# Optimization experiments

Hardware: AMD Instinct MI355X
Metric: run time of the kernel (lower is better)

## Reference

```python
import jax, jax.numpy as jnp
import numpy as np

NUM_EXPERTS = 8
TOP_K = 2
N_EMBD = 1024
D_FFN = 2048  # 4*N_EMBD // TOP_K, already multiple of BLOCK_N=128
BLOCK_M = 128
NORM_TOPK = True


def setup_inputs() -> dict:
    key = jax.random.key(0)
    k1, k2, k3 = jax.random.split(key, 3)
    x = jax.random.normal(k1, (2, 2048, N_EMBD), dtype=jnp.float32)
    router_w = jax.random.normal(k2, (NUM_EXPERTS, N_EMBD), dtype=jnp.float32) * 0.02
    w1 = jax.random.normal(k3, (N_EMBD, D_FFN * NUM_EXPERTS), dtype=jnp.float32) * 0.02
    return {"x": x, "router_w": router_w, "w1": w1}


def reference(x, router_w, w1):
    B, S, H = x.shape
    x_flat = x.reshape(-1, H)                                   # [T, H]
    router_logits = x_flat @ router_w.T                         # [T, E]
    probs = jax.nn.softmax(router_logits.astype(jnp.float32), axis=-1)
    rweights, sel = jax.lax.top_k(probs, TOP_K)                 # [T, k]
    if NORM_TOPK:
        rweights = rweights / rweights.sum(axis=-1, keepdims=True)
    rweights = rweights.astype(x.dtype)

    # repeat_interleave tokens top_k times, then stable-sort by expert id
    x_rep = jnp.repeat(x_flat, TOP_K, axis=0)                   # [M, H]
    sel_rep = sel.reshape(-1)                                   # [M]
    rw_rep = rweights.reshape(-1, 1)                            # [M, 1]
    order = jnp.argsort(sel_rep, stable=True)                   # expert-sort permutation
    x_grouped = x_rep[order]                                    # [M, H]
    sel_sorted = sel_rep[order]                                 # [M]
    rw_sorted = rw_rep[order]                                   # [M, 1]

    M = x_grouped.shape[0]
    nblk = M // BLOCK_M                                         # M divisible by BLOCK_M by construction
    # SDD kernel: expert of the first row of each BLOCK_M block selects w1 slice
    block_expert = sel_sorted[::BLOCK_M]                        # [nblk] == col_indices_ptr
    w1e = w1.reshape(H, NUM_EXPERTS, D_FFN)                     # w1[:, e*D:(e+1)*D] == w1e[:, e, :]
    w_blk = jnp.take(w1e, block_expert, axis=1)                 # [H, nblk, D]
    x_blk = x_grouped.reshape(nblk, BLOCK_M, H)                 # [nblk, Bm, H]
    block_sparse = jnp.einsum('bmh,hbd->bmd', x_blk, w_blk).reshape(M, D_FFN)

    block_sparse = jax.nn.gelu(block_sparse, approximate=False) * rw_sorted
    return block_sparse, router_logits
```

## Files before the change

kernel.cpp:

```cpp
#include <hip/hip_runtime.h>
#include <hip/hip_bf16.h>
#include <cmath>

typedef float f32x16 __attribute__((ext_vector_type(16)));
typedef __bf16 bf16x8 __attribute__((ext_vector_type(8)));
typedef __bf16 bf16x4 __attribute__((ext_vector_type(4)));

#define NE 8
#define H 1024
#define DF 2048
#define WCOLS 16384
#define NTOK 4096
#define MROWS 8192
#define NBLK 64
#define TILE_E 4096

typedef const __attribute__((address_space(1))) unsigned int glb_u32;
typedef __attribute__((address_space(3))) unsigned int lds_u32;

__device__ __forceinline__ void async_load16(const void* g, void* l) {
    __builtin_amdgcn_global_load_lds((glb_u32*)g, (lds_u32*)l, 16, 0, 0);
}

__global__ __launch_bounds__(256) void prep_kernel(
    const float* __restrict__ x, const float* __restrict__ rw,
    const float* __restrict__ w1,
    float* __restrict__ logits, int* __restrict__ sel, float* __restrict__ rwn,
    __bf16* __restrict__ xb, __bf16* __restrict__ Wt)
{
    __shared__ float tile[32][132];
    int b = blockIdx.x;
    int tid = threadIdx.x;
    if (b < 1024) {
        int tok  = b * 4 + (tid >> 6);
        int lane = tid & 63;
        const float* xr = x + (size_t)tok * H;
        __bf16* xbr = xb + (size_t)tok * H;
        float acc[NE];
#pragma unroll
        for (int e = 0; e < NE; ++e) acc[e] = 0.f;
#pragma unroll
        for (int it = 0; it < 4; ++it) {
            int k = (it * 64 + lane) * 4;
            float4 xv = *(const float4*)(xr + k);
            bf16x4 xc;
            xc[0] = (__bf16)xv.x; xc[1] = (__bf16)xv.y;
            xc[2] = (__bf16)xv.z; xc[3] = (__bf16)xv.w;
            *(bf16x4*)(xbr + k) = xc;
#pragma unroll
            for (int e = 0; e < NE; ++e) {
                float4 wv = *(const float4*)(rw + e * H + k);
                acc[e] += xv.x * wv.x + xv.y * wv.y + xv.z * wv.z + xv.w * wv.w;
            }
        }
#pragma unroll
        for (int e = 0; e < NE; ++e) {
            float v = acc[e];
#pragma unroll
            for (int off = 32; off > 0; off >>= 1) v += __shfl_xor(v, off, 64);
            acc[e] = v;
        }
        if (lane == 0) {
#pragma unroll
            for (int e = 0; e < NE; ++e) logits[tok * NE + e] = acc[e];
            int i1 = 0; float m1 = acc[0];
#pragma unroll
            for (int e = 1; e < NE; ++e) if (acc[e] > m1) { m1 = acc[e]; i1 = e; }
            int i2 = -1; float m2 = -INFINITY;
#pragma unroll
            for (int e = 0; e < NE; ++e) if (e != i1 && acc[e] > m2) { m2 = acc[e]; i2 = e; }
            float e2 = expf(m2 - m1);
            float inv = 1.f / (1.f + e2);
            sel[tok * 2]     = i1;  sel[tok * 2 + 1] = i2;
            rwn[tok * 2]     = inv; rwn[tok * 2 + 1] = e2 * inv;
        }
        return;
    }
    int g  = b - 1024;
    int c  = g >> 5;
    int kb = g & 31;
    int kk = tid >> 3;
    int cc = (tid & 7) * 16;
    const float* src = w1 + (size_t)(kb * 32 + kk) * WCOLS + c * 128 + cc;
#pragma unroll
    for (int i = 0; i < 4; ++i) {
        float4 v = *(const float4*)(src + i * 4);
        *(float4*)&tile[kk][cc + i * 4] = v;
    }
    __syncthreads();
    int n = tid >> 1, kc0 = (tid & 1) * 16;
    bf16x8 o0, o1;
#pragma unroll
    for (int i = 0; i < 8; ++i) {
        o0[i] = (__bf16)tile[kc0 + i][n];
        o1[i] = (__bf16)tile[kc0 + 8 + i][n];
    }
    __bf16* dst = Wt + (size_t)g * TILE_E + n * 32 + kc0;
    *(bf16x8*)dst       = o0;
    *(bf16x8*)(dst + 8) = o1;
}

__global__ __launch_bounds__(1024) void sort_kernel(
    const int* __restrict__ sel, const float* __restrict__ rwn,
    int* __restrict__ stok, float* __restrict__ srw, int* __restrict__ bexp)
{
    __shared__ int cnt[NE][1024];
    __shared__ int wtot[NE][2];
    __shared__ int ebase[NE + 1];
    int t = threadIdx.x;
    int selv[8];
    int lc[NE];
#pragma unroll
    for (int e = 0; e < NE; ++e) lc[e] = 0;
    int base = t * 8;
#pragma unroll
    for (int j = 0; j < 8; ++j) { selv[j] = sel[base + j]; lc[selv[j]]++; }
#pragma unroll
    for (int e = 0; e < NE; ++e) cnt[e][t] = lc[e];
    __syncthreads();
    int g = t >> 7, j = t & 127, jl = j & 63;
    int s = 0, pre[8];
#pragma unroll
    for (int i = 0; i < 8; ++i) { pre[i] = s; s += cnt[g][j * 8 + i]; }
    int inc = s;
#pragma unroll
    for (int d = 1; d < 64; d <<= 1) {
        int v = __shfl_up(inc, d, 64);
        if (jl >= d) inc += v;
    }
    if (jl == 63) wtot[g][j >> 6] = inc;
    __syncthreads();
    int add = (j >= 64) ? wtot[g][0] : 0;
    int excl = inc - s + add;
#pragma unroll
    for (int i = 0; i < 8; ++i) cnt[g][j * 8 + i] = excl + pre[i];
    __syncthreads();
    if (t == 0) {
        int acc = 0;
        for (int e = 0; e < NE; ++e) { ebase[e] = acc; acc += wtot[e][0] + wtot[e][1]; }
        ebase[NE] = acc;
    }
    __syncthreads();
    int off[NE];
#pragma unroll
    for (int e = 0; e < NE; ++e) off[e] = ebase[e] + cnt[e][t];
#pragma unroll
    for (int j2 = 0; j2 < 8; ++j2) {
        int i = base + j2;
        int e = selv[j2];
        int pos = off[e]++;
        stok[pos] = i >> 1;
        srw[pos]  = rwn[i];
    }
    __syncthreads();
    if (t < NBLK) {
        int r = t * 128;
        int e = 0;
        while (e < NE - 1 && r >= ebase[e + 1]) ++e;
        bexp[t] = e;
    }
}

__global__ __launch_bounds__(256, 4) void moe_gemm(
    const __bf16* __restrict__ xb, const __bf16* __restrict__ Wt,
    const int* __restrict__ stok, const float* __restrict__ srw,
    const int* __restrict__ bexp, float* __restrict__ out)
{
    __shared__ __align__(16) __bf16 As[2][4096];
    __shared__ __align__(16) __bf16 Bs[2][4096];
    __shared__ int   tokS[128];
    __shared__ float rwS[128];

    int g = blockIdx.x;
    int by = (g & 7) * 8 + ((g >> 3) & 7);
    int bx = g >> 6;
    int tid = threadIdx.x;
    if (tid < 128) {
        tokS[tid] = stok[by * 128 + tid];
        rwS[tid]  = srw[by * 128 + tid];
    }
    int e = bexp[by];
    __syncthreads();

    int lane = tid & 63;
    int wv   = tid >> 6;
    int rsub = lane >> 2;
    int kcE  = (lane & 3) * 8;
    int r0   = wv * 32 + rsub;
    int r1   = r0 + 16;

    const __bf16* aS0 = xb + (size_t)tokS[r0] * H + kcE;
    const __bf16* aS1 = xb + (size_t)tokS[r1] * H + kcE;
    const __bf16* bT  = Wt + (size_t)(e * 16 + bx) * 32 * TILE_E + wv * 1024 + lane * 8;
    __bf16* aL[2] = { &As[0][wv * 1024], &As[1][wv * 1024] };
    __bf16* bL[2] = { &Bs[0][wv * 1024], &Bs[1][wv * 1024] };

    int wm  = (wv & 1) * 64;
    int wn  = (wv >> 1) * 64;
    int l32 = lane & 31;
    int khi = (lane >> 5) * 8;

    f32x16 acc[2][2];
#pragma unroll
    for (int i = 0; i < 2; ++i)
#pragma unroll
        for (int j = 0; j < 2; ++j)
#pragma unroll
            for (int r = 0; r < 16; ++r) acc[i][j][r] = 0.f;

    async_load16(aS0, aL[0]);
    async_load16(aS1, aL[0] + 512);
    async_load16(bT,  bL[0]);
    async_load16(bT + 512, bL[0] + 512);

    for (int kb = 0; kb < 32; ++kb) {
        int cur = kb & 1;
        __syncthreads();
        if (kb < 31) {
            const __bf16* aN0 = aS0 + (kb + 1) * 32;
            const __bf16* aN1 = aS1 + (kb + 1) * 32;
            const __bf16* bN  = bT + (size_t)(kb + 1) * TILE_E;
            async_load16(aN0, aL[1 - cur]);
            async_load16(aN1, aL[1 - cur] + 512);
            async_load16(bN,  bL[1 - cur]);
            async_load16(bN + 512, bL[1 - cur] + 512);
        }
        bf16x8 af[2][2], bfr[2][2];
#pragma unroll
        for (int h = 0; h < 2; ++h) {
#pragma unroll
            for (int ti = 0; ti < 2; ++ti)
                af[ti][h] = *(const bf16x8*)&As[cur][(wm + ti * 32 + l32) * 32 + h * 16 + khi];
#pragma unroll
            for (int tj = 0; tj < 2; ++tj)
                bfr[tj][h] = *(const bf16x8*)&Bs[cur][(wn + tj * 32 + l32) * 32 + h * 16 + khi];
        }
#pragma unroll
        for (int h = 0; h < 2; ++h)
#pragma unroll
            for (int ti = 0; ti < 2; ++ti)
#pragma unroll
                for (int tj = 0; tj < 2; ++tj)
                    acc[ti][tj] = __builtin_amdgcn_mfma_f32_32x32x16_bf16(
                        af[ti][h], bfr[tj][h], acc[ti][tj], 0, 0, 0);
    }

    int rowh = (lane >> 5) * 4;
#pragma unroll
    for (int ti = 0; ti < 2; ++ti)
#pragma unroll
        for (int tj = 0; tj < 2; ++tj)
#pragma unroll
            for (int reg = 0; reg < 16; ++reg) {
                int row = (reg & 3) + 8 * (reg >> 2) + rowh;
                int m = wm + ti * 32 + row;
                int n = wn + tj * 32 + l32;
                float val = acc[ti][tj][reg];
                float u = 0.7978845608028654f * val * (1.f + 0.044715f * val * val);
                float t = __expf(-2.f * fabsf(u));
                float th = (1.f - t) / (1.f + t);
                th = u < 0.f ? -th : th;
                float gv = 0.5f * val * (1.f + th) * rwS[m];
                out[(size_t)(by * 128 + m) * DF + bx * 128 + n] = gv;
            }
}

extern "C" void kernel_launch(void* const* d_in, const int* in_sizes, int n_in,
                              void* d_out, int out_size, void* d_ws, size_t ws_size,
                              hipStream_t stream) {
    (void)in_sizes; (void)n_in; (void)out_size; (void)ws_size;
    const float* x        = (const float*)d_in[0];
    const float* router_w = (const float*)d_in[1];
    const float* w1       = (const float*)d_in[2];
    float* out    = (float*)d_out;
    float* logits = out + (size_t)MROWS * DF;

    char* ws    = (char*)d_ws;
    int*   sel  = (int*)(ws);
    float* rwn  = (float*)(ws + 0x8000);
    int*   stok = (int*)(ws + 0x10000);
    float* srw  = (float*)(ws + 0x18000);
    int*   bexp = (int*)(ws + 0x20000);
    __bf16* xb  = (__bf16*)(ws + (1 << 20));
    __bf16* Wt  = (__bf16*)(ws + (1 << 20) + (8 << 20));

    prep_kernel<<<5120, 256, 0, stream>>>(x, router_w, w1, logits, sel, rwn, xb, Wt);
    sort_kernel<<<1, 1024, 0, stream>>>(sel, rwn, stok, srw, bexp);
    moe_gemm<<<16 * NBLK, 256, 0, stream>>>(xb, Wt, stok, srw, bexp, out);
}
```

Measured before the change: 189.1 us.

## Fuse expert sort into prep via last-block atomic, relayout W tiles

Removes the separate single-block sort kernel by having the last router block, detected with an atomic counter, perform the counting sort inside the prep kernel. The W1 transpose-convert no longer uses LDS staging: each thread gathers 8 strided fp32 values and writes bf16x8, and the grid doubles to cover the work. The A and B LDS layouts are changed to match the MFMA fragment reads, presumably to cut LDS bank conflicts. This adds a memset launch and a serialized sort tail in one block, and the strided global reads of w1 may coalesce poorly.

```diff
diff --git a/kernel.cpp b/kernel.cpp
--- a/kernel.cpp
+++ b/kernel.cpp
@@ -26,12 +26,28 @@
     const float* __restrict__ x, const float* __restrict__ rw,
     const float* __restrict__ w1,
     float* __restrict__ logits, int* __restrict__ sel, float* __restrict__ rwn,
-    __bf16* __restrict__ xb, __bf16* __restrict__ Wt)
+    __bf16* __restrict__ xb, __bf16* __restrict__ Wt,
+    int* __restrict__ ctr,
+    int* __restrict__ stok, float* __restrict__ srw, int* __restrict__ bexp)
 {
-    __shared__ float tile[32][132];
     int b = blockIdx.x;
     int tid = threadIdx.x;
-    if (b < 1024) {
+    if (b >= 1024) {
+        int gblk = b - 1024;
+        int pair = gblk >> 1;
+        int c  = pair >> 5;
+        int kb = pair & 31;
+        int g4 = (gblk & 1) * 2 + (tid >> 7);
+        int ch = (tid >> 5) & 3;
+        int r32 = tid & 31;
+        const float* src = w1 + (size_t)(kb * 32 + ch * 8) * WCOLS + c * 128 + g4 * 32 + r32;
+        bf16x8 o;
+#pragma unroll
+        for (int j = 0; j < 8; ++j) o[j] = (__bf16)src[(size_t)j * WCOLS];
+        *(bf16x8*)(Wt + (size_t)pair * TILE_E + g4 * 1024 + ch * 256 + r32 * 8) = o;
+        return;
+    }
+    {
         int tok  = b * 4 + (tid >> 6);
         int lane = tid & 63;
         const float* xr = x + (size_t)tok * H;
@@ -74,80 +90,60 @@
             sel[tok * 2]     = i1;  sel[tok * 2 + 1] = i2;
             rwn[tok * 2]     = inv; rwn[tok * 2 + 1] = e2 * inv;
         }
-        return;
-    }
-    int g  = b - 1024;
-    int c  = g >> 5;
-    int kb = g & 31;
-    int kk = tid >> 3;
-    int cc = (tid & 7) * 16;
-    const float* src = w1 + (size_t)(kb * 32 + kk) * WCOLS + c * 128 + cc;
-#pragma unroll
-    for (int i = 0; i < 4; ++i) {
-        float4 v = *(const float4*)(src + i * 4);
-        *(float4*)&tile[kk][cc + i * 4] = v;
-    }
-    __syncthreads();
-    int n = tid >> 1, kc0 = (tid & 1) * 16;
-    bf16x8 o0, o1;
-#pragma unroll
-    for (int i = 0; i < 8; ++i) {
-        o0[i] = (__bf16)tile[kc0 + i][n];
-        o1[i] = (__bf16)tile[kc0 + 8 + i][n];
-    }
-    __bf16* dst = Wt + (size_t)g * TILE_E + n * 32 + kc0;
-    *(bf16x8*)dst       = o0;
-    *(bf16x8*)(dst + 8) = o1;
-}
-
-__global__ __launch_bounds__(1024) void sort_kernel(
-    const int* __restrict__ sel, const float* __restrict__ rwn,
-    int* __restrict__ stok, float* __restrict__ srw, int* __restrict__ bexp)
-{
-    __shared__ int cnt[NE][1024];
-    __shared__ int wtot[NE][2];
+    }
+    __shared__ int lastFlag;
+    __syncthreads();
+    if (tid == 0) {
+        __threadfence();
+        int old = atomicAdd(ctr, 1);
+        lastFlag = (old == 1023) ? 1 : 0;
+    }
+    __syncthreads();
+    if (!lastFlag) return;
+    __threadfence();
+
+    __shared__ int cnt[NE][256];
+    __shared__ int tot[NE];
     __shared__ int ebase[NE + 1];
-    int t = threadIdx.x;
-    int selv[8];
+    int t = tid;
+    int selv[32];
     int lc[NE];
 #pragma unroll
     for (int e = 0; e < NE; ++e) lc[e] = 0;
-    int base = t * 8;
-#pragma unroll
-    for (int j = 0; j < 8; ++j) { selv[j] = sel[base + j]; lc[selv[j]]++; }
+    int base = t * 32;
+    for (int j = 0; j < 32; ++j) { selv[j] = sel[base + j]; lc[selv[j]]++; }
 #pragma unroll
     for (int e = 0; e < NE; ++e) cnt[e][t] = lc[e];
     __syncthreads();
-    int g = t >> 7, j = t & 127, jl = j & 63;
-    int s = 0, pre[8];
-#pragma unroll
-    for (int i = 0; i < 8; ++i) { pre[i] = s; s += cnt[g][j * 8 + i]; }
-    int inc = s;
-#pragma unroll
-    for (int d = 1; d < 64; d <<= 1) {
-        int v = __shfl_up(inc, d, 64);
-        if (jl >= d) inc += v;
-    }
-    if (jl == 63) wtot[g][j >> 6] = inc;
-    __syncthreads();
-    int add = (j >= 64) ? wtot[g][0] : 0;
-    int excl = inc - s + add;
-#pragma unroll
-    for (int i = 0; i < 8; ++i) cnt[g][j * 8 + i] = excl + pre[i];
+    {
+        int gg = t >> 5, j = t & 31;
+        int s = 0, pre[8];
+#pragma unroll
+        for (int i = 0; i < 8; ++i) { pre[i] = s; s += cnt[gg][j * 8 + i]; }
+        int inc = s;
+#pragma unroll
+        for (int d = 1; d < 32; d <<= 1) {
+            int v = __shfl_up(inc, d, 64);
+            if (j >= d) inc += v;
+        }
+        int excl = inc - s;
+#pragma unroll
+        for (int i = 0; i < 8; ++i) cnt[gg][j * 8 + i] = excl + pre[i];
+        if (j == 31) tot[gg] = inc;
+    }
     __syncthreads();
     if (t == 0) {
-        int acc = 0;
-        for (int e = 0; e < NE; ++e) { ebase[e] = acc; acc += wtot[e][0] + wtot[e][1]; }
-        ebase[NE] = acc;
+        int s = 0;
+        for (int e = 0; e < NE; ++e) { ebase[e] = s; s += tot[e]; }
+        ebase[NE] = s;
     }
     __syncthreads();
     int off[NE];
 #pragma unroll
     for (int e = 0; e < NE; ++e) off[e] = ebase[e] + cnt[e][t];
-#pragma unroll
-    for (int j2 = 0; j2 < 8; ++j2) {
-        int i = base + j2;
-        int e = selv[j2];
+    for (int j = 0; j < 32; ++j) {
+        int i = base + j;
+        int e = selv[j];
         int pos = off[e]++;
         stok[pos] = i >> 1;
         srw[pos]  = rwn[i];
@@ -184,21 +180,20 @@
 
     int lane = tid & 63;
     int wv   = tid >> 6;
-    int rsub = lane >> 2;
-    int kcE  = (lane & 3) * 8;
-    int r0   = wv * 32 + rsub;
-    int r1   = r0 + 16;
-
-    const __bf16* aS0 = xb + (size_t)tokS[r0] * H + kcE;
-    const __bf16* aS1 = xb + (size_t)tokS[r1] * H + kcE;
+    int r16  = lane & 15;
+    int ch4  = lane >> 4;
+    const __bf16* aS0 = xb + (size_t)tokS[wv * 32 + r16] * H + ch4 * 8;
+    const __bf16* aS1 = xb + (size_t)tokS[wv * 32 + 16 + r16] * H + ch4 * 8;
     const __bf16* bT  = Wt + (size_t)(e * 16 + bx) * 32 * TILE_E + wv * 1024 + lane * 8;
-    __bf16* aL[2] = { &As[0][wv * 1024], &As[1][wv * 1024] };
-    __bf16* bL[2] = { &Bs[0][wv * 1024], &Bs[1][wv * 1024] };
-
-    int wm  = (wv & 1) * 64;
-    int wn  = (wv >> 1) * 64;
+
     int l32 = lane & 31;
-    int khi = (lane >> 5) * 8;
+    int hi  = lane >> 5;
+    int rgA0 = (wv & 1) * 2;
+    int rgB0 = (wv >> 1) * 2;
+    int aoff = (l32 >> 4) * 512 + hi * 128 + (l32 & 15) * 8;
+    int boff = hi * 256 + l32 * 8;
+    int wm = (wv & 1) * 64;
+    int wn = (wv >> 1) * 64;
 
     f32x16 acc[2][2];
 #pragma unroll
@@ -208,10 +203,10 @@
 #pragma unroll
             for (int r = 0; r < 16; ++r) acc[i][j][r] = 0.f;
 
-    async_load16(aS0, aL[0]);
-    async_load16(aS1, aL[0] + 512);
-    async_load16(bT,  bL[0]);
-    async_load16(bT + 512, bL[0] + 512);
+    async_load16(aS0, &As[0][wv * 1024]);
+    async_load16(aS1, &As[0][wv * 1024 + 512]);
+    async_load16(bT,  &Bs[0][wv * 1024]);
+    async_load16(bT + 512, &Bs[0][wv * 1024 + 512]);
 
     for (int kb = 0; kb < 32; ++kb) {
         int cur = kb & 1;
@@ -220,20 +215,20 @@
             const __bf16* aN0 = aS0 + (kb + 1) * 32;
             const __bf16* aN1 = aS1 + (kb + 1) * 32;
             const __bf16* bN  = bT + (size_t)(kb + 1) * TILE_E;
-            async_load16(aN0, aL[1 - cur]);
-            async_load16(aN1, aL[1 - cur] + 512);
-            async_load16(bN,  bL[1 - cur]);
-            async_load16(bN + 512, bL[1 - cur] + 512);
+            async_load16(aN0, &As[1 - cur][wv * 1024]);
+            async_load16(aN1, &As[1 - cur][wv * 1024 + 512]);
+            async_load16(bN,  &Bs[1 - cur][wv * 1024]);
+            async_load16(bN + 512, &Bs[1 - cur][wv * 1024 + 512]);
         }
         bf16x8 af[2][2], bfr[2][2];
 #pragma unroll
         for (int h = 0; h < 2; ++h) {
 #pragma unroll
             for (int ti = 0; ti < 2; ++ti)
-                af[ti][h] = *(const bf16x8*)&As[cur][(wm + ti * 32 + l32) * 32 + h * 16 + khi];
+                af[ti][h] = *(const bf16x8*)&As[cur][(rgA0 + ti) * 1024 + h * 256 + aoff];
 #pragma unroll
             for (int tj = 0; tj < 2; ++tj)
-                bfr[tj][h] = *(const bf16x8*)&Bs[cur][(wn + tj * 32 + l32) * 32 + h * 16 + khi];
+                bfr[tj][h] = *(const bf16x8*)&Bs[cur][(rgB0 + tj) * 1024 + h * 512 + boff];
         }
 #pragma unroll
         for (int h = 0; h < 2; ++h)
@@ -245,7 +240,7 @@
                         af[ti][h], bfr[tj][h], acc[ti][tj], 0, 0, 0);
     }
 
-    int rowh = (lane >> 5) * 4;
+    int rowh = hi * 4;
 #pragma unroll
     for (int ti = 0; ti < 2; ++ti)
 #pragma unroll
@@ -281,10 +276,12 @@
     int*   stok = (int*)(ws + 0x10000);
     float* srw  = (float*)(ws + 0x18000);
     int*   bexp = (int*)(ws + 0x20000);
+    int*   ctr  = (int*)(ws + 0x21000);
     __bf16* xb  = (__bf16*)(ws + (1 << 20));
     __bf16* Wt  = (__bf16*)(ws + (1 << 20) + (8 << 20));
 
-    prep_kernel<<<5120, 256, 0, stream>>>(x, router_w, w1, logits, sel, rwn, xb, Wt);
-    sort_kernel<<<1, 1024, 0, stream>>>(sel, rwn, stok, srw, bexp);
+    hipMemsetAsync(ctr, 0, 4, stream);
+    prep_kernel<<<9216, 256, 0, stream>>>(x, router_w, w1, logits, sel, rwn,
+                                          xb, Wt, ctr, stok, srw, bexp);
     moe_gemm<<<16 * NBLK, 256, 0, stream>>>(xb, Wt, stok, srw, bexp, out);
 }
```

Result: slower. 237.1 us (+25.4%).
